# Kernel tuning notes

Hardware: AMD Instinct MI355X
Metric: run time of the kernel (lower is better)

## Reference

```python
import jax, jax.numpy as jnp
import numpy as np

HIDDEN = 64

def setup_inputs() -> dict:
    key = jax.random.key(0)
    ks = jax.random.split(key, 6)
    inp = {
        "input_a": jax.random.normal(ks[0], (16, 6209, 256), dtype=jnp.float32),
        "input_b": jax.random.normal(ks[1], (16, 256, 256), dtype=jnp.float32),
        # Linear weights stored as [in, out]; xavier-ish scale
        "Wa": jax.random.normal(ks[2], (256, HIDDEN), dtype=jnp.float32) * (2.0 / (256 + HIDDEN)) ** 0.5,
        "ba": jnp.zeros((HIDDEN,), dtype=jnp.float32),
        "Wb": jax.random.normal(ks[3], (256, HIDDEN), dtype=jnp.float32) * (2.0 / (256 + HIDDEN)) ** 0.5,
        "bb": jnp.zeros((HIDDEN,), dtype=jnp.float32),
        "Wc": jax.random.normal(ks[4], (HIDDEN, 256), dtype=jnp.float32) * (2.0 / (HIDDEN + 256)) ** 0.5,
        "bc": jnp.zeros((256,), dtype=jnp.float32),
    }
    return inp

def reference(input_a, input_b, Wa, ba, Wb, bb, Wc, bc):
    # mapped_a: [b, dima, h], mapped_b: [b, dimb, h]
    mapped_a = jnp.einsum("bif,fh->bih", input_a, Wa) + ba
    mapped_b = jnp.einsum("bjf,fh->bjh", input_b, Wb) + bb
    # NOTE: original divides by scale = hidden**-0.5, i.e. multiplies by sqrt(hidden)
    scores = jnp.einsum("bih,bjh->bij", mapped_a, mapped_b) * jnp.sqrt(jnp.float32(HIDDEN))
    attn = jax.nn.softmax(scores, axis=-1)  # dropout is identity in eval
    out = jnp.einsum("bij,bjh->bih", attn, mapped_b)
    out = jnp.einsum("bih,hf->bif", out, Wc) + bc
    return out
```

## Files before the change

### kernel.cpp

```cpp
#include <hip/hip_runtime.h>

typedef float f32x4 __attribute__((ext_vector_type(4)));
typedef short s16x8 __attribute__((ext_vector_type(8)));

#define MFMA16(a, b, c) __builtin_amdgcn_mfma_f32_16x16x32_bf16((a), (b), (c), 0, 0, 0)

#define B_ 16
#define M_ 6209
#define F_ 256
#define NTR_ 389
#define NT_ 392

static __device__ __forceinline__ unsigned short f2bf(float x) {
    unsigned u = __builtin_bit_cast(unsigned, x);
    unsigned r = u + 0x7fffu + ((u >> 16) & 1u);
    return (unsigned short)(r >> 16);
}
static __device__ __forceinline__ float bf2f(unsigned short h) {
    unsigned u = ((unsigned)h) << 16;
    return __builtin_bit_cast(float, u);
}
static __device__ __forceinline__ void split_bf(float x, unsigned short& hi, unsigned short& lo) {
    hi = f2bf(x);
    lo = f2bf(x - bf2f(hi));
}
static __device__ __forceinline__ unsigned cvtpk_bf16(float a, float b) {
    unsigned r;
    asm("v_cvt_pk_bf16_f32 %0, %1, %2" : "=v"(r) : "v"(a), "v"(b));
    return r;
}

#define SW64(row, k)  ((row) * 64 + ((k) ^ (((row) & 7) << 3)))
#define SW256(row, k) ((row) * 256 + ((k) ^ (((row) & 7) << 3)))

__global__ void k_mapped_b(const float* __restrict__ inB, const float* __restrict__ Wb,
                           const float* __restrict__ bb, float* __restrict__ mb) {
    int bj = blockIdx.x;
    int b = bj >> 8, j = bj & 255;
    __shared__ float row[256];
    int t = threadIdx.x;
    const float* src = inB + ((size_t)(b * 256 + j)) * 256;
    for (int i = t; i < 256; i += 64) row[i] = src[i];
    __syncthreads();
    float s = bb[t];
    #pragma unroll 8
    for (int f = 0; f < 256; ++f) s = fmaf(row[f], Wb[f * 64 + t], s);
    mb[(size_t)(b * 256 + j) * 64 + t] = s;
}

__global__ void k_pack(const float* __restrict__ mb, const float* __restrict__ Wa,
                       const float* __restrict__ Wc,
                       unsigned short* __restrict__ waf_hi, unsigned short* __restrict__ waf_lo,
                       unsigned short* __restrict__ wcf,
                       unsigned short* __restrict__ mbb_hi, unsigned short* __restrict__ mbb_lo,
                       unsigned short* __restrict__ mbp) {
    int idx = blockIdx.x * 256 + threadIdx.x;
    if (idx < 16384) {
        int i = idx;
        int jj = i & 7, lane = (i >> 3) & 63, nf = (i >> 9) & 3, ks = i >> 11;
        int g = lane >> 4, c = lane & 15;
        int f = ks * 32 + g * 8 + jj, h = nf * 16 + c;
        unsigned short hi, lo; split_bf(Wa[f * 64 + h], hi, lo);
        waf_hi[i] = hi; waf_lo[i] = lo;
    } else if (idx < 32768) {
        int i = idx - 16384;
        int jj = i & 7, lane = (i >> 3) & 63, nf = (i >> 9) & 15, ks = i >> 13;
        int g = lane >> 4, c = lane & 15;
        int h = ks * 32 + g * 8 + jj, f = nf * 16 + c;
        wcf[i] = f2bf(Wc[h * 256 + f]);
    } else if (idx < 32768 + 262144) {
        int i = idx - 32768;
        int jj = i & 7, lane = (i >> 3) & 63, nf = (i >> 9) & 15, ks = (i >> 13) & 1, b = i >> 14;
        int g = lane >> 4, c = lane & 15;
        int h = ks * 32 + g * 8 + jj, j = nf * 16 + c;
        unsigned short hi, lo; split_bf(mb[((size_t)(b * 256 + j)) * 64 + h], hi, lo);
        mbb_hi[i] = hi; mbb_lo[i] = lo;
    } else {
        int i = idx - (32768 + 262144);
        int jj = i & 7, lane = (i >> 3) & 63, nf = (i >> 9) & 3, ks = (i >> 11) & 7, b = i >> 14;
        int g = lane >> 4, c = lane & 15;
        int j = ks * 32 + g * 8 + jj, h = nf * 16 + c;
        mbp[i] = f2bf(mb[((size_t)(b * 256 + j)) * 64 + h]);
    }
}

__global__ __launch_bounds__(256) void k_ma(
    const float* __restrict__ A, const float* __restrict__ ba,
    const unsigned short* __restrict__ waf_hi, const unsigned short* __restrict__ waf_lo,
    unsigned short* __restrict__ mafh, unsigned short* __restrict__ mafl) {
    __shared__ __align__(16) unsigned short maH[4][1024];
    __shared__ __align__(16) unsigned short maL[4][1024];
    const int w = threadIdx.x >> 6, lane = threadIdx.x & 63;
    const int g = lane >> 4, c = lane & 15;
    const int t = blockIdx.x * 4 + w, b = blockIdx.y;

    f32x4 accA[4];
    #pragma unroll
    for (int nf = 0; nf < 4; ++nf) { float v = ba[nf * 16 + c]; accA[nf] = (f32x4){v, v, v, v}; }
    int arow = t * 16 + c; if (arow > M_ - 1) arow = M_ - 1;
    const float* abase = A + ((size_t)b * M_ + arow) * F_;
    #pragma unroll
    for (int ks = 0; ks < 8; ++ks) {
        const f32x4 a0 = *(const f32x4*)(abase + ks * 32 + g * 8);
        const f32x4 a1 = *(const f32x4*)(abase + ks * 32 + g * 8 + 4);
        s16x8 ah, al;
        #pragma unroll
        for (int j = 0; j < 4; ++j) {
            unsigned short hi, lo;
            split_bf(a0[j], hi, lo); ah[j] = (short)hi; al[j] = (short)lo;
            split_bf(a1[j], hi, lo); ah[4 + j] = (short)hi; al[4 + j] = (short)lo;
        }
        #pragma unroll
        for (int nf = 0; nf < 4; ++nf) {
            const int off = ((ks * 4 + nf) * 64 + lane) << 3;
            const s16x8 bh = *(const s16x8*)(waf_hi + off);
            const s16x8 bl = *(const s16x8*)(waf_lo + off);
            accA[nf] = MFMA16(ah, bh, accA[nf]);
            accA[nf] = MFMA16(ah, bl, accA[nf]);
            accA[nf] = MFMA16(al, bh, accA[nf]);
        }
    }
    #pragma unroll
    for (int nf = 0; nf < 4; ++nf) {
        #pragma unroll
        for (int r = 0; r < 4; ++r) {
            unsigned short hi, lo; split_bf(accA[nf][r], hi, lo);
            const int idx = SW64(g * 4 + r, nf * 16 + c);
            maH[w][idx] = hi; maL[w][idx] = lo;
        }
    }
    __syncthreads();
    #pragma unroll
    for (int ks = 0; ks < 2; ++ks) {
        const s16x8 fh = *(const s16x8*)&maH[w][SW64(c, ks * 32 + g * 8)];
        const s16x8 fl = *(const s16x8*)&maL[w][SW64(c, ks * 32 + g * 8)];
        const size_t off = (((size_t)(b * NT_ + t) * 2 + ks) * 64 + lane) << 3;
        *(s16x8*)(mafh + off) = fh;
        *(s16x8*)(mafl + off) = fl;
    }
}

__global__ __launch_bounds__(256) void k_attn(
    const unsigned short* __restrict__ mafh, const unsigned short* __restrict__ mafl,
    const unsigned short* __restrict__ mbb_hi, const unsigned short* __restrict__ mbb_lo,
    const unsigned short* __restrict__ mbp, const unsigned short* __restrict__ wcf,
    const float* __restrict__ bc, float* __restrict__ out) {
    __shared__ __align__(16) unsigned short pSh[16 * 256];
    __shared__ __align__(16) unsigned short o1S[16 * 64];
    __shared__ float pmaxS[4][16];
    __shared__ float psumS[4][16];

    const int t = blockIdx.x, b = blockIdx.y;
    const int w = threadIdx.x >> 6, lane = threadIdx.x & 63;
    const int g = lane >> 4, c = lane & 15;
    const int q0 = t * 16;
    const float SC = 11.541560327f;

    s16x8 bh[2], bl[2];
    #pragma unroll
    for (int ks = 0; ks < 2; ++ks) {
        const size_t off = (((size_t)(b * NT_ + t) * 2 + ks) * 64 + lane) << 3;
        bh[ks] = *(const s16x8*)(mafh + off);
        bl[ks] = *(const s16x8*)(mafl + off);
    }

    f32x4 accST[4];
    #pragma unroll
    for (int jtl = 0; jtl < 4; ++jtl) accST[jtl] = (f32x4){0.f, 0.f, 0.f, 0.f};
    #pragma unroll
    for (int jtl = 0; jtl < 4; ++jtl) {
        const int jt = w * 4 + jtl;
        const size_t off0 = ((((size_t)b * 2 + 0) * 16 + jt) * 64 + lane) << 3;
        const size_t off1 = ((((size_t)b * 2 + 1) * 16 + jt) * 64 + lane) << 3;
        const s16x8 ah0 = *(const s16x8*)(mbb_hi + off0);
        const s16x8 al0 = *(const s16x8*)(mbb_lo + off0);
        const s16x8 ah1 = *(const s16x8*)(mbb_hi + off1);
        const s16x8 al1 = *(const s16x8*)(mbb_lo + off1);
        f32x4 acc = accST[jtl];
        acc = MFMA16(ah0, bh[0], acc);
        acc = MFMA16(ah1, bh[1], acc);
        acc = MFMA16(ah0, bl[0], acc);
        acc = MFMA16(ah1, bl[1], acc);
        acc = MFMA16(al0, bh[0], acc);
        acc = MFMA16(al1, bh[1], acc);
        accST[jtl] = acc;
    }

    float m = accST[0][0];
    #pragma unroll
    for (int jtl = 0; jtl < 4; ++jtl) {
        m = fmaxf(m, accST[jtl][0]); m = fmaxf(m, accST[jtl][1]);
        m = fmaxf(m, accST[jtl][2]); m = fmaxf(m, accST[jtl][3]);
    }
    m = fmaxf(m, __shfl_xor(m, 16));
    m = fmaxf(m, __shfl_xor(m, 32));
    if (lane < 16) pmaxS[w][lane] = m;
    __syncthreads();

    const float mg = fmaxf(fmaxf(pmaxS[0][c], pmaxS[1][c]),
                           fmaxf(pmaxS[2][c], pmaxS[3][c]));
    float s = 0.f;
    #pragma unroll
    for (int jtl = 0; jtl < 4; ++jtl) {
        f32x4 p;
        #pragma unroll
        for (int r = 0; r < 4; ++r) {
            p[r] = __builtin_amdgcn_exp2f((accST[jtl][r] - mg) * SC);
            s += p[r];
        }
        const unsigned w0 = cvtpk_bf16(p[0], p[1]);
        const unsigned w1 = cvtpk_bf16(p[2], p[3]);
        const unsigned long long wv = (unsigned long long)w0 | ((unsigned long long)w1 << 32);
        *(unsigned long long*)&pSh[SW256(c, (w * 4 + jtl) * 16 + g * 4)] = wv;
    }
    s += __shfl_xor(s, 16);
    s += __shfl_xor(s, 32);
    if (lane < 16) psumS[w][lane] = s;
    __syncthreads();

    f32x4 acc1 = (f32x4){0.f, 0.f, 0.f, 0.f};
    #pragma unroll
    for (int ks = 0; ks < 8; ++ks) {
        const s16x8 pf = *(const s16x8*)&pSh[SW256(c, ks * 32 + g * 8)];
        const size_t off = ((((size_t)b * 8 + ks) * 4 + w) * 64 + lane) << 3;
        const s16x8 av = *(const s16x8*)(mbp + off);
        acc1 = MFMA16(av, pf, acc1);
    }
    const float rinv = 1.f / (psumS[0][c] + psumS[1][c] + psumS[2][c] + psumS[3][c]);
    {
        const unsigned w0 = cvtpk_bf16(acc1[0] * rinv, acc1[1] * rinv);
        const unsigned w1 = cvtpk_bf16(acc1[2] * rinv, acc1[3] * rinv);
        const unsigned long long wv = (unsigned long long)w0 | ((unsigned long long)w1 << 32);
        *(unsigned long long*)&o1S[SW64(c, w * 16 + g * 4)] = wv;
    }
    __syncthreads();

    s16x8 af[2];
    #pragma unroll
    for (int ks = 0; ks < 2; ++ks)
        af[ks] = *(const s16x8*)&o1S[SW64(c, ks * 32 + g * 8)];
    #pragma unroll
    for (int ftl = 0; ftl < 4; ++ftl) {
        const int ft = w * 4 + ftl;
        const float bv = bc[ft * 16 + c];
        f32x4 acc = (f32x4){bv, bv, bv, bv};
        const s16x8 wb0 = *(const s16x8*)(wcf + (((0 * 16 + ft) * 64 + lane) << 3));
        const s16x8 wb1 = *(const s16x8*)(wcf + (((1 * 16 + ft) * 64 + lane) << 3));
        acc = MFMA16(af[0], wb0, acc);
        acc = MFMA16(af[1], wb1, acc);
        #pragma unroll
        for (int r = 0; r < 4; ++r) {
            const int q = q0 + g * 4 + r;
            if (q < M_) out[((size_t)b * M_ + q) * F_ + ft * 16 + c] = acc[r];
        }
    }
}

extern "C" void kernel_launch(void* const* d_in, const int* in_sizes, int n_in,
                              void* d_out, int out_size, void* d_ws, size_t ws_size,
                              hipStream_t stream) {
    (void)in_sizes; (void)n_in; (void)out_size; (void)ws_size;
    const float* inA = (const float*)d_in[0];
    const float* inB = (const float*)d_in[1];
    const float* Wa  = (const float*)d_in[2];
    const float* ba  = (const float*)d_in[3];
    const float* Wb  = (const float*)d_in[4];
    const float* bb  = (const float*)d_in[5];
    const float* Wc  = (const float*)d_in[6];
    const float* bc  = (const float*)d_in[7];
    float* out = (float*)d_out;

    char* ws = (char*)d_ws;
    float* mb              = (float*)ws;
    unsigned short* waf_hi = (unsigned short*)(ws + 1048576);
    unsigned short* waf_lo = (unsigned short*)(ws + 1081344);
    unsigned short* wcf    = (unsigned short*)(ws + 1114112);
    unsigned short* mbb_hi = (unsigned short*)(ws + 1146880);
    unsigned short* mbb_lo = (unsigned short*)(ws + 1671168);
    unsigned short* mbp    = (unsigned short*)(ws + 2195456);
    unsigned short* mafh   = (unsigned short*)(ws + 2719744);
    unsigned short* mafl   = (unsigned short*)(ws + 15564800);

    hipLaunchKernelGGL(k_mapped_b, dim3(B_ * 256), dim3(64), 0, stream, inB, Wb, bb, mb);
    hipLaunchKernelGGL(k_pack, dim3((557056 + 255) / 256), dim3(256), 0, stream,
                       mb, Wa, Wc, waf_hi, waf_lo, wcf, mbb_hi, mbb_lo, mbp);
    hipLaunchKernelGGL(k_ma, dim3(98, B_), dim3(256), 0, stream,
                       inA, ba, waf_hi, waf_lo, mafh, mafl);
    hipLaunchKernelGGL(k_attn, dim3(NTR_, B_), dim3(256), 0, stream,
                       mafh, mafl, mbb_hi, mbb_lo, mbp, wcf, bc, out);
}
```

Before: 92.53 us.

## Merge prep kernels and process two query tiles per wave in projection and attention

Fuses the mapped_b projection and weight packing into one prep kernel, and folds mb packing into the A-projection launch, cutting four launches to three. The A-projection now computes two 16-row tiles per wave, so the Wa fragments it loads are reused across both. The attention kernel now handles two query tiles per block, so the mapped_b and Wc fragments are loaded once and used twice. The cost is more registers and shared memory per block, and the attention grid shrinks to half as many blocks. The mapped_b projection also now reads input rows with vector loads.

```diff
diff --git a/kernel.cpp b/kernel.cpp
--- a/kernel.cpp
+++ b/kernel.cpp
@@ -33,140 +33,171 @@
 #define SW64(row, k)  ((row) * 64 + ((k) ^ (((row) & 7) << 3)))
 #define SW256(row, k) ((row) * 256 + ((k) ^ (((row) & 7) << 3)))
 
-__global__ void k_mapped_b(const float* __restrict__ inB, const float* __restrict__ Wb,
-                           const float* __restrict__ bb, float* __restrict__ mb) {
-    int bj = blockIdx.x;
-    int b = bj >> 8, j = bj & 255;
-    __shared__ float row[256];
-    int t = threadIdx.x;
-    const float* src = inB + ((size_t)(b * 256 + j)) * 256;
-    for (int i = t; i < 256; i += 64) row[i] = src[i];
-    __syncthreads();
-    float s = bb[t];
-    #pragma unroll 8
-    for (int f = 0; f < 256; ++f) s = fmaf(row[f], Wb[f * 64 + t], s);
-    mb[(size_t)(b * 256 + j) * 64 + t] = s;
-}
-
-__global__ void k_pack(const float* __restrict__ mb, const float* __restrict__ Wa,
-                       const float* __restrict__ Wc,
-                       unsigned short* __restrict__ waf_hi, unsigned short* __restrict__ waf_lo,
-                       unsigned short* __restrict__ wcf,
-                       unsigned short* __restrict__ mbb_hi, unsigned short* __restrict__ mbb_lo,
-                       unsigned short* __restrict__ mbp) {
-    int idx = blockIdx.x * 256 + threadIdx.x;
-    if (idx < 16384) {
-        int i = idx;
-        int jj = i & 7, lane = (i >> 3) & 63, nf = (i >> 9) & 3, ks = i >> 11;
-        int g = lane >> 4, c = lane & 15;
-        int f = ks * 32 + g * 8 + jj, h = nf * 16 + c;
-        unsigned short hi, lo; split_bf(Wa[f * 64 + h], hi, lo);
-        waf_hi[i] = hi; waf_lo[i] = lo;
-    } else if (idx < 32768) {
-        int i = idx - 16384;
-        int jj = i & 7, lane = (i >> 3) & 63, nf = (i >> 9) & 15, ks = i >> 13;
-        int g = lane >> 4, c = lane & 15;
-        int h = ks * 32 + g * 8 + jj, f = nf * 16 + c;
-        wcf[i] = f2bf(Wc[h * 256 + f]);
-    } else if (idx < 32768 + 262144) {
-        int i = idx - 32768;
-        int jj = i & 7, lane = (i >> 3) & 63, nf = (i >> 9) & 15, ks = (i >> 13) & 1, b = i >> 14;
-        int g = lane >> 4, c = lane & 15;
-        int h = ks * 32 + g * 8 + jj, j = nf * 16 + c;
-        unsigned short hi, lo; split_bf(mb[((size_t)(b * 256 + j)) * 64 + h], hi, lo);
-        mbb_hi[i] = hi; mbb_lo[i] = lo;
+__global__ __launch_bounds__(256) void k_prep(
+    const float* __restrict__ inB, const float* __restrict__ Wb, const float* __restrict__ bb,
+    const float* __restrict__ Wa, const float* __restrict__ Wc,
+    float* __restrict__ mb,
+    unsigned short* __restrict__ waf_hi, unsigned short* __restrict__ waf_lo,
+    unsigned short* __restrict__ wcf) {
+    const int blk = blockIdx.x;
+    if (blk < 1024) {
+        const int b = blk >> 6;
+        const int j = (blk & 63) * 4 + (threadIdx.x >> 6);
+        const int h = threadIdx.x & 63;
+        const float* src = inB + ((size_t)(b * 256 + j)) * 256;
+        float s = bb[h];
+        #pragma unroll 4
+        for (int f4 = 0; f4 < 64; ++f4) {
+            const f32x4 v = *(const f32x4*)(src + f4 * 4);
+            s = fmaf(v[0], Wb[(f4 * 4 + 0) * 64 + h], s);
+            s = fmaf(v[1], Wb[(f4 * 4 + 1) * 64 + h], s);
+            s = fmaf(v[2], Wb[(f4 * 4 + 2) * 64 + h], s);
+            s = fmaf(v[3], Wb[(f4 * 4 + 3) * 64 + h], s);
+        }
+        mb[((size_t)(b * 256 + j)) * 64 + h] = s;
     } else {
-        int i = idx - (32768 + 262144);
-        int jj = i & 7, lane = (i >> 3) & 63, nf = (i >> 9) & 3, ks = (i >> 11) & 7, b = i >> 14;
-        int g = lane >> 4, c = lane & 15;
-        int j = ks * 32 + g * 8 + jj, h = nf * 16 + c;
-        mbp[i] = f2bf(mb[((size_t)(b * 256 + j)) * 64 + h]);
-    }
-}
-
-__global__ __launch_bounds__(256) void k_ma(
+        const int idx = (blk - 1024) * 256 + threadIdx.x;
+        if (idx < 16384) {
+            int i = idx;
+            int jj = i & 7, lane = (i >> 3) & 63, nf = (i >> 9) & 3, ks = i >> 11;
+            int g = lane >> 4, c = lane & 15;
+            int f = ks * 32 + g * 8 + jj, h = nf * 16 + c;
+            unsigned short hi, lo; split_bf(Wa[f * 64 + h], hi, lo);
+            waf_hi[i] = hi; waf_lo[i] = lo;
+        } else {
+            int i = idx - 16384;
+            int jj = i & 7, lane = (i >> 3) & 63, nf = (i >> 9) & 15, ks = i >> 13;
+            int g = lane >> 4, c = lane & 15;
+            int h = ks * 32 + g * 8 + jj, f = nf * 16 + c;
+            wcf[i] = f2bf(Wc[h * 256 + f]);
+        }
+    }
+}
+
+__global__ __launch_bounds__(256, 3) void k_mapk(
     const float* __restrict__ A, const float* __restrict__ ba,
     const unsigned short* __restrict__ waf_hi, const unsigned short* __restrict__ waf_lo,
+    const float* __restrict__ mb,
+    unsigned short* __restrict__ mbb_hi, unsigned short* __restrict__ mbb_lo,
+    unsigned short* __restrict__ mbp,
     unsigned short* __restrict__ mafh, unsigned short* __restrict__ mafl) {
-    __shared__ __align__(16) unsigned short maH[4][1024];
-    __shared__ __align__(16) unsigned short maL[4][1024];
-    const int w = threadIdx.x >> 6, lane = threadIdx.x & 63;
-    const int g = lane >> 4, c = lane & 15;
-    const int t = blockIdx.x * 4 + w, b = blockIdx.y;
-
-    f32x4 accA[4];
-    #pragma unroll
-    for (int nf = 0; nf < 4; ++nf) { float v = ba[nf * 16 + c]; accA[nf] = (f32x4){v, v, v, v}; }
-    int arow = t * 16 + c; if (arow > M_ - 1) arow = M_ - 1;
-    const float* abase = A + ((size_t)b * M_ + arow) * F_;
-    #pragma unroll
-    for (int ks = 0; ks < 8; ++ks) {
-        const f32x4 a0 = *(const f32x4*)(abase + ks * 32 + g * 8);
-        const f32x4 a1 = *(const f32x4*)(abase + ks * 32 + g * 8 + 4);
-        s16x8 ah, al;
-        #pragma unroll
-        for (int j = 0; j < 4; ++j) {
-            unsigned short hi, lo;
-            split_bf(a0[j], hi, lo); ah[j] = (short)hi; al[j] = (short)lo;
-            split_bf(a1[j], hi, lo); ah[4 + j] = (short)hi; al[4 + j] = (short)lo;
-        }
-        #pragma unroll
-        for (int nf = 0; nf < 4; ++nf) {
-            const int off = ((ks * 4 + nf) * 64 + lane) << 3;
-            const s16x8 bh = *(const s16x8*)(waf_hi + off);
-            const s16x8 bl = *(const s16x8*)(waf_lo + off);
-            accA[nf] = MFMA16(ah, bh, accA[nf]);
-            accA[nf] = MFMA16(ah, bl, accA[nf]);
-            accA[nf] = MFMA16(al, bh, accA[nf]);
-        }
-    }
-    #pragma unroll
-    for (int nf = 0; nf < 4; ++nf) {
-        #pragma unroll
-        for (int r = 0; r < 4; ++r) {
-            unsigned short hi, lo; split_bf(accA[nf][r], hi, lo);
-            const int idx = SW64(g * 4 + r, nf * 16 + c);
-            maH[w][idx] = hi; maL[w][idx] = lo;
-        }
-    }
-    __syncthreads();
-    #pragma unroll
-    for (int ks = 0; ks < 2; ++ks) {
-        const s16x8 fh = *(const s16x8*)&maH[w][SW64(c, ks * 32 + g * 8)];
-        const s16x8 fl = *(const s16x8*)&maL[w][SW64(c, ks * 32 + g * 8)];
-        const size_t off = (((size_t)(b * NT_ + t) * 2 + ks) * 64 + lane) << 3;
-        *(s16x8*)(mafh + off) = fh;
-        *(s16x8*)(mafl + off) = fl;
-    }
-}
-
-__global__ __launch_bounds__(256) void k_attn(
+    __shared__ __align__(16) unsigned short maH[4][2][1024];
+    __shared__ __align__(16) unsigned short maL[4][2][1024];
+    const int blk = blockIdx.x;
+    if (blk < 784) {
+        const int b = blk / 49, bx = blk % 49;
+        const int w = threadIdx.x >> 6, lane = threadIdx.x & 63;
+        const int g = lane >> 4, c = lane & 15;
+        const int t0 = (bx * 4 + w) * 2;
+
+        f32x4 accA[2][4];
+        #pragma unroll
+        for (int i = 0; i < 2; ++i)
+            #pragma unroll
+            for (int nf = 0; nf < 4; ++nf) { float v = ba[nf * 16 + c]; accA[i][nf] = (f32x4){v, v, v, v}; }
+        const float* ab[2];
+        #pragma unroll
+        for (int i = 0; i < 2; ++i) {
+            int arow = (t0 + i) * 16 + c; if (arow > M_ - 1) arow = M_ - 1;
+            ab[i] = A + ((size_t)b * M_ + arow) * F_;
+        }
+        #pragma unroll
+        for (int ks = 0; ks < 8; ++ks) {
+            s16x8 ah[2], al[2];
+            #pragma unroll
+            for (int i = 0; i < 2; ++i) {
+                const f32x4 a0 = *(const f32x4*)(ab[i] + ks * 32 + g * 8);
+                const f32x4 a1 = *(const f32x4*)(ab[i] + ks * 32 + g * 8 + 4);
+                #pragma unroll
+                for (int j = 0; j < 4; ++j) {
+                    unsigned short hi, lo;
+                    split_bf(a0[j], hi, lo); ah[i][j] = (short)hi; al[i][j] = (short)lo;
+                    split_bf(a1[j], hi, lo); ah[i][4 + j] = (short)hi; al[i][4 + j] = (short)lo;
+                }
+            }
+            #pragma unroll
+            for (int nf = 0; nf < 4; ++nf) {
+                const int off = ((ks * 4 + nf) * 64 + lane) << 3;
+                const s16x8 bh = *(const s16x8*)(waf_hi + off);
+                const s16x8 bl = *(const s16x8*)(waf_lo + off);
+                #pragma unroll
+                for (int i = 0; i < 2; ++i) {
+                    accA[i][nf] = MFMA16(ah[i], bh, accA[i][nf]);
+                    accA[i][nf] = MFMA16(ah[i], bl, accA[i][nf]);
+                    accA[i][nf] = MFMA16(al[i], bh, accA[i][nf]);
+                }
+            }
+        }
+        #pragma unroll
+        for (int i = 0; i < 2; ++i)
+            #pragma unroll
+            for (int nf = 0; nf < 4; ++nf)
+                #pragma unroll
+                for (int r = 0; r < 4; ++r) {
+                    unsigned short hi, lo; split_bf(accA[i][nf][r], hi, lo);
+                    const int idx = SW64(g * 4 + r, nf * 16 + c);
+                    maH[w][i][idx] = hi; maL[w][i][idx] = lo;
+                }
+        __syncthreads();
+        #pragma unroll
+        for (int i = 0; i < 2; ++i)
+            #pragma unroll
+            for (int ks = 0; ks < 2; ++ks) {
+                const s16x8 fh = *(const s16x8*)&maH[w][i][SW64(c, ks * 32 + g * 8)];
+                const s16x8 fl = *(const s16x8*)&maL[w][i][SW64(c, ks * 32 + g * 8)];
+                const size_t off = (((size_t)(b * NT_ + t0 + i) * 2 + ks) * 64 + lane) << 3;
+                *(s16x8*)(mafh + off) = fh;
+                *(s16x8*)(mafl + off) = fl;
+            }
+    } else {
+        const int i2 = (blk - 784) * 256 + threadIdx.x;
+        if (i2 < 262144) {
+            int i = i2;
+            int jj = i & 7, lane = (i >> 3) & 63, nf = (i >> 9) & 15, ks = (i >> 13) & 1, b = i >> 14;
+            int g = lane >> 4, c = lane & 15;
+            int h = ks * 32 + g * 8 + jj, j = nf * 16 + c;
+            unsigned short hi, lo; split_bf(mb[((size_t)(b * 256 + j)) * 64 + h], hi, lo);
+            mbb_hi[i] = hi; mbb_lo[i] = lo;
+        } else {
+            int i = i2 - 262144;
+            int jj = i & 7, lane = (i >> 3) & 63, nf = (i >> 9) & 3, ks = (i >> 11) & 7, b = i >> 14;
+            int g = lane >> 4, c = lane & 15;
+            int j = ks * 32 + g * 8 + jj, h = nf * 16 + c;
+            mbp[i] = f2bf(mb[((size_t)(b * 256 + j)) * 64 + h]);
+        }
+    }
+}
+
+__global__ __launch_bounds__(256, 4) void k_attn2(
     const unsigned short* __restrict__ mafh, const unsigned short* __restrict__ mafl,
     const unsigned short* __restrict__ mbb_hi, const unsigned short* __restrict__ mbb_lo,
     const unsigned short* __restrict__ mbp, const unsigned short* __restrict__ wcf,
     const float* __restrict__ bc, float* __restrict__ out) {
-    __shared__ __align__(16) unsigned short pSh[16 * 256];
-    __shared__ __align__(16) unsigned short o1S[16 * 64];
-    __shared__ float pmaxS[4][16];
-    __shared__ float psumS[4][16];
-
-    const int t = blockIdx.x, b = blockIdx.y;
+    __shared__ __align__(16) unsigned short pSh[2][16 * 256];
+    __shared__ __align__(16) unsigned short o1S[2][16 * 64];
+    __shared__ float pmaxS[2][4][16];
+    __shared__ float psumS[2][4][16];
+
+    const int t0 = blockIdx.x * 2, b = blockIdx.y;
     const int w = threadIdx.x >> 6, lane = threadIdx.x & 63;
     const int g = lane >> 4, c = lane & 15;
-    const int q0 = t * 16;
     const float SC = 11.541560327f;
 
-    s16x8 bh[2], bl[2];
-    #pragma unroll
-    for (int ks = 0; ks < 2; ++ks) {
-        const size_t off = (((size_t)(b * NT_ + t) * 2 + ks) * 64 + lane) << 3;
-        bh[ks] = *(const s16x8*)(mafh + off);
-        bl[ks] = *(const s16x8*)(mafl + off);
-    }
-
-    f32x4 accST[4];
-    #pragma unroll
-    for (int jtl = 0; jtl < 4; ++jtl) accST[jtl] = (f32x4){0.f, 0.f, 0.f, 0.f};
+    s16x8 bh[2][2], bl[2][2];
+    #pragma unroll
+    for (int i = 0; i < 2; ++i)
+        #pragma unroll
+        for (int ks = 0; ks < 2; ++ks) {
+            const size_t off = (((size_t)(b * NT_ + t0 + i) * 2 + ks) * 64 + lane) << 3;
+            bh[i][ks] = *(const s16x8*)(mafh + off);
+            bl[i][ks] = *(const s16x8*)(mafl + off);
+        }
+
+    f32x4 accST[2][4];
+    #pragma unroll
+    for (int i = 0; i < 2; ++i)
+        #pragma unroll
+        for (int jtl = 0; jtl < 4; ++jtl) accST[i][jtl] = (f32x4){0.f, 0.f, 0.f, 0.f};
     #pragma unroll
     for (int jtl = 0; jtl < 4; ++jtl) {
         const int jt = w * 4 + jtl;
@@ -176,82 +207,100 @@
         const s16x8 al0 = *(const s16x8*)(mbb_lo + off0);
         const s16x8 ah1 = *(const s16x8*)(mbb_hi + off1);
         const s16x8 al1 = *(const s16x8*)(mbb_lo + off1);
-        f32x4 acc = accST[jtl];
-        acc = MFMA16(ah0, bh[0], acc);
-        acc = MFMA16(ah1, bh[1], acc);
-        acc = MFMA16(ah0, bl[0], acc);
-        acc = MFMA16(ah1, bl[1], acc);
-        acc = MFMA16(al0, bh[0], acc);
-        acc = MFMA16(al1, bh[1], acc);
-        accST[jtl] = acc;
-    }
-
-    float m = accST[0][0];
-    #pragma unroll
-    for (int jtl = 0; jtl < 4; ++jtl) {
-        m = fmaxf(m, accST[jtl][0]); m = fmaxf(m, accST[jtl][1]);
-        m = fmaxf(m, accST[jtl][2]); m = fmaxf(m, accST[jtl][3]);
-    }
-    m = fmaxf(m, __shfl_xor(m, 16));
-    m = fmaxf(m, __shfl_xor(m, 32));
-    if (lane < 16) pmaxS[w][lane] = m;
+        #pragma unroll
+        for (int i = 0; i < 2; ++i) {
+            f32x4 acc = accST[i][jtl];
+            acc = MFMA16(ah0, bh[i][0], acc);
+            acc = MFMA16(ah1, bh[i][1], acc);
+            acc = MFMA16(ah0, bl[i][0], acc);
+            acc = MFMA16(ah1, bl[i][1], acc);
+            acc = MFMA16(al0, bh[i][0], acc);
+            acc = MFMA16(al1, bh[i][1], acc);
+            accST[i][jtl] = acc;
+        }
+    }
+
+    #pragma unroll
+    for (int i = 0; i < 2; ++i) {
+        float m = accST[i][0][0];
+        #pragma unroll
+        for (int jtl = 0; jtl < 4; ++jtl) {
+            m = fmaxf(m, accST[i][jtl][0]); m = fmaxf(m, accST[i][jtl][1]);
+            m = fmaxf(m, accST[i][jtl][2]); m = fmaxf(m, accST[i][jtl][3]);
+        }
+        m = fmaxf(m, __shfl_xor(m, 16));
+        m = fmaxf(m, __shfl_xor(m, 32));
+        if (lane < 16) pmaxS[i][w][lane] = m;
+    }
     __syncthreads();
 
-    const float mg = fmaxf(fmaxf(pmaxS[0][c], pmaxS[1][c]),
-                           fmaxf(pmaxS[2][c], pmaxS[3][c]));
-    float s = 0.f;
-    #pragma unroll
-    for (int jtl = 0; jtl < 4; ++jtl) {
-        f32x4 p;
-        #pragma unroll
-        for (int r = 0; r < 4; ++r) {
-            p[r] = __builtin_amdgcn_exp2f((accST[jtl][r] - mg) * SC);
-            s += p[r];
-        }
-        const unsigned w0 = cvtpk_bf16(p[0], p[1]);
-        const unsigned w1 = cvtpk_bf16(p[2], p[3]);
-        const unsigned long long wv = (unsigned long long)w0 | ((unsigned long long)w1 << 32);
-        *(unsigned long long*)&pSh[SW256(c, (w * 4 + jtl) * 16 + g * 4)] = wv;
-    }
-    s += __shfl_xor(s, 16);
-    s += __shfl_xor(s, 32);
-    if (lane < 16) psumS[w][lane] = s;
+    #pragma unroll
+    for (int i = 0; i < 2; ++i) {
+        const float mg = fmaxf(fmaxf(pmaxS[i][0][c], pmaxS[i][1][c]),
+                               fmaxf(pmaxS[i][2][c], pmaxS[i][3][c]));
+        float s = 0.f;
+        #pragma unroll
+        for (int jtl = 0; jtl < 4; ++jtl) {
+            f32x4 p;
+            #pragma unroll
+            for (int r = 0; r < 4; ++r) {
+                p[r] = __builtin_amdgcn_exp2f((accST[i][jtl][r] - mg) * SC);
+                s += p[r];
+            }
+            const unsigned w0 = cvtpk_bf16(p[0], p[1]);
+            const unsigned w1 = cvtpk_bf16(p[2], p[3]);
+            const unsigned long long wv = (unsigned long long)w0 | ((unsigned long long)w1 << 32);
+            *(unsigned long long*)&pSh[i][SW256(c, (w * 4 + jtl) * 16 + g * 4)] = wv;
+        }
+        s += __shfl_xor(s, 16);
+        s += __shfl_xor(s, 32);
+        if (lane < 16) psumS[i][w][lane] = s;
+    }
     __syncthreads();
 
-    f32x4 acc1 = (f32x4){0.f, 0.f, 0.f, 0.f};
+    f32x4 acc1[2] = {(f32x4){0.f, 0.f, 0.f, 0.f}, (f32x4){0.f, 0.f, 0.f, 0.f}};
     #pragma unroll
     for (int ks = 0; ks < 8; ++ks) {
-        const s16x8 pf = *(const s16x8*)&pSh[SW256(c, ks * 32 + g * 8)];
         const size_t off = ((((size_t)b * 8 + ks) * 4 + w) * 64 + lane) << 3;
         const s16x8 av = *(const s16x8*)(mbp + off);
-        acc1 = MFMA16(av, pf, acc1);
-    }
-    const float rinv = 1.f / (psumS[0][c] + psumS[1][c] + psumS[2][c] + psumS[3][c]);
-    {
-        const unsigned w0 = cvtpk_bf16(acc1[0] * rinv, acc1[1] * rinv);
-        const unsigned w1 = cvtpk_bf16(acc1[2] * rinv, acc1[3] * rinv);
+        #pragma unroll
+        for (int i = 0; i < 2; ++i) {
+            const s16x8 pf = *(const s16x8*)&pSh[i][SW256(c, ks * 32 + g * 8)];
+            acc1[i] = MFMA16(av, pf, acc1[i]);
+        }
+    }
+    #pragma unroll
+    for (int i = 0; i < 2; ++i) {
+        const float rinv = 1.f / (psumS[i][0][c] + psumS[i][1][c] + psumS[i][2][c] + psumS[i][3][c]);
+        const unsigned w0 = cvtpk_bf16(acc1[i][0] * rinv, acc1[i][1] * rinv);
+        const unsigned w1 = cvtpk_bf16(acc1[i][2] * rinv, acc1[i][3] * rinv);
         const unsigned long long wv = (unsigned long long)w0 | ((unsigned long long)w1 << 32);
-        *(unsigned long long*)&o1S[SW64(c, w * 16 + g * 4)] = wv;
+        *(unsigned long long*)&o1S[i][SW64(c, w * 16 + g * 4)] = wv;
     }
     __syncthreads();
 
-    s16x8 af[2];
-    #pragma unroll
-    for (int ks = 0; ks < 2; ++ks)
-        af[ks] = *(const s16x8*)&o1S[SW64(c, ks * 32 + g * 8)];
+    s16x8 af[2][2];
+    #pragma unroll
+    for (int i = 0; i < 2; ++i)
+        #pragma unroll
+        for (int ks = 0; ks < 2; ++ks)
+            af[i][ks] = *(const s16x8*)&o1S[i][SW64(c, ks * 32 + g * 8)];
     #pragma unroll
     for (int ftl = 0; ftl < 4; ++ftl) {
         const int ft = w * 4 + ftl;
         const float bv = bc[ft * 16 + c];
-        f32x4 acc = (f32x4){bv, bv, bv, bv};
         const s16x8 wb0 = *(const s16x8*)(wcf + (((0 * 16 + ft) * 64 + lane) << 3));
         const s16x8 wb1 = *(const s16x8*)(wcf + (((1 * 16 + ft) * 64 + lane) << 3));
-        acc = MFMA16(af[0], wb0, acc);
-        acc = MFMA16(af[1], wb1, acc);
-        #pragma unroll
-        for (int r = 0; r < 4; ++r) {
-            const int q = q0 + g * 4 + r;
-            if (q < M_) out[((size_t)b * M_ + q) * F_ + ft * 16 + c] = acc[r];
+        #pragma unroll
+        for (int i = 0; i < 2; ++i) {
+            f32x4 acc = (f32x4){bv, bv, bv, bv};
+            acc = MFMA16(af[i][0], wb0, acc);
+            acc = MFMA16(af[i][1], wb1, acc);
+            #pragma unroll
+            for (int r = 0; r < 4; ++r) {
+                const int q = (t0 + i) * 16 + g * 4 + r;
+                if (q < M_) out[((size_t)b * M_ + q) * F_ + ft * 16 + c] = acc[r];
+            }
         }
     }
 }
@@ -281,11 +330,10 @@
     unsigned short* mafh   = (unsigned short*)(ws + 2719744);
     unsigned short* mafl   = (unsigned short*)(ws + 15564800);
 
-    hipLaunchKernelGGL(k_mapped_b, dim3(B_ * 256), dim3(64), 0, stream, inB, Wb, bb, mb);
-    hipLaunchKernelGGL(k_pack, dim3((557056 + 255) / 256), dim3(256), 0, stream,
-                       mb, Wa, Wc, waf_hi, waf_lo, wcf, mbb_hi, mbb_lo, mbp);
-    hipLaunchKernelGGL(k_ma, dim3(98, B_), dim3(256), 0, stream,
-                       inA, ba, waf_hi, waf_lo, mafh, mafl);
-    hipLaunchKernelGGL(k_attn, dim3(NTR_, B_), dim3(256), 0, stream,
+    hipLaunchKernelGGL(k_prep, dim3(1024 + 128), dim3(256), 0, stream,
+                       inB, Wb, bb, Wa, Wc, mb, waf_hi, waf_lo, wcf);
+    hipLaunchKernelGGL(k_mapk, dim3(784 + 2048), dim3(256), 0, stream,
+                       inA, ba, waf_hi, waf_lo, mb, mbb_hi, mbb_lo, mbp, mafh, mafl);
+    hipLaunchKernelGGL(k_attn2, dim3(195, B_), dim3(256), 0, stream,
                        mafh, mafl, mbb_hi, mbb_lo, mbp, wcf, bc, out);
 }
```

After: 81.88 us. 1.13x faster.
